# Performance work log

Measured on AMD Instinct MI355X. Metric: run time of the kernel, lower is better.

Reference implementation:

```python
import jax, jax.numpy as jnp
import numpy as np
from jax import lax

HID = 128  # hidden_dim
K = 2      # kernel (must be 2 for the torch slice arithmetic to be shape-consistent)


def skew(x):
    # x: (B,C,H,W) -> (B,C,H,2W-1), row r shifted right by r
    B, C, H, W = x.shape
    rows = jnp.arange(H)[:, None]
    cols = jnp.arange(W)[None, :] + rows
    y = jnp.zeros((B, C, H, 2 * W - 1), x.dtype)
    return y.at[:, :, rows, cols].set(x)


def unskew(x):
    B, C, H, Wp = x.shape
    W = (Wp + 1) // 2
    rows = jnp.arange(H)[:, None]
    cols = jnp.arange(W)[None, :] + rows
    return x[:, :, rows, cols]


def setup_inputs() -> dict:
    key = jax.random.key(0)
    k1, k2, k3 = jax.random.split(key, 3)
    Cin = 128
    x = jax.random.normal(k1, (8, Cin, 64, 64), jnp.float32)
    w_is = jax.random.normal(k2, (4 * HID, Cin), jnp.float32) * 0.05   # 1x1 conv weight
    b_is = jnp.zeros((4 * HID,), jnp.float32)
    w_ss = jax.random.normal(k3, (4 * HID, HID, K, 1), jnp.float32) * 0.05  # (k,1) conv weight
    b_ss = jnp.zeros((4 * HID,), jnp.float32)
    return {"x": x, "w_is": w_is, "b_is": b_is, "w_ss": w_ss, "b_ss": b_ss}


def reference(x, w_is, b_is, w_ss, b_ss):
    B, Cin, H, W = x.shape
    hid, k = HID, K
    xs = skew(x)  # (B,Cin,H,2W-1)
    # input-to-state: 1x1 conv (mask B on 1x1 kernel == plain 1x1 conv)
    z_is = jnp.einsum('bchw,oc->bohw', xs, w_is) + b_is[None, :, None, None]
    steps = z_is.transpose(3, 0, 1, 2)  # (2W-1, B, 4hid, H)

    h0 = jnp.zeros((B, hid, H), x.dtype)
    c0 = jnp.zeros((B, hid, H), x.dtype)

    def step(carry, z_t):
        h, c = carry  # (B,hid,H)
        # state-to-state (k,1) conv along H, padding k//2, then drop last k-1 rows
        hs = lax.conv_general_dilated(h[..., None], w_ss, (1, 1),
                                      [(k // 2, k // 2), (0, 0)],
                                      dimension_numbers=('NCHW', 'OIHW', 'NCHW'))
        hs = hs[:, :, :-(k - 1), 0] + b_ss[None, :, None]  # (B,4hid,H)
        z = z_t + hs
        i = jax.nn.sigmoid(z[:, :hid])
        f = jax.nn.sigmoid(z[:, hid:2 * hid])
        o = jax.nn.sigmoid(z[:, 2 * hid:3 * hid])
        g = jnp.tanh(z[:, 3 * hid:])
        c = f * c + i * g
        h = o * jnp.tanh(c)
        return (h, c), h

    _, hs_all = lax.scan(step, (h0, c0), steps)  # (2W-1,B,hid,H)
    out = hs_all.transpose(1, 2, 3, 0)  # (B,hid,H,2W-1)
    return unskew(out)  # (B,hid,H,W)
```

## Files before the change

kernel.cpp:

```cpp
#include <hip/hip_runtime.h>
#include <hip/hip_fp16.h>
#include <math.h>


#define HID 128
#define BB 8
#define HH 64
#define WW 64
#define TT 127

#define NPREP 1022

#define HROW 136

typedef _Float16 v8h __attribute__((ext_vector_type(8)));
typedef float v4f __attribute__((ext_vector_type(4)));

#define SENT64 0xFFFFFFFFFFFFFFFFULL

__device__ __forceinline__ float fsig(float x) {
  float e = __builtin_amdgcn_exp2f(x * -1.44269504f);
  return __builtin_amdgcn_rcpf(1.f + e);
}
__device__ __forceinline__ float ftanh_(float x) {
  float e = __builtin_amdgcn_exp2f(x * 2.88539009f);
  return __builtin_fmaf(-2.f, __builtin_amdgcn_rcpf(1.f + e), 1.f);
}

__global__ __launch_bounds__(256) void prep_k(
    const float* __restrict__ w_ss, const float* __restrict__ b_is,
    const float* __restrict__ b_ss, _Float16* __restrict__ wp,
    __half* __restrict__ zph, unsigned long long* __restrict__ hx) {
  int idx = blockIdx.x * 256 + threadIdx.x;
  if (idx < 131072) {
    int j = idx & 7;
    int L = (idx >> 3) & 63;
    int kt = (idx >> 9) & 7;
    int mt = idx >> 12;
    int O = mt * 16 + (L & 15);
    int k = kt * 32 + ((L >> 4) & 3) * 8 + j;
    float v = (k < 128) ? w_ss[(size_t)O * 256 + k * 2]
                        : w_ss[(size_t)O * 256 + (k - 128) * 2 + 1];
    wp[idx] = (_Float16)v;
  } else if (idx < 131584) {
    int idx2 = idx - 131072;
    int g = (idx2 >> 2) & 3;
    int u = (idx2 >> 4) * 4 + (idx2 & 3);
    int O = g * 128 + u;
    zph[(size_t)BB * HH * WW * 512 + idx2] = __float2half(b_is[O] + b_ss[O]);
  } else {
    int j = idx - 131584;
    uint4 s;
    s.x = 0xFFFFFFFFu; s.y = 0xFFFFFFFFu;
    s.z = 0xFFFFFFFFu; s.w = 0xFFFFFFFFu;
    ((uint4*)hx)[j] = s;
  }
}

#define STEP_BARRIER()                                   \
  do {                                                   \
    asm volatile("s_waitcnt lgkmcnt(0)" ::: "memory");   \
    __builtin_amdgcn_s_barrier();                        \
    asm volatile("" ::: "memory");                       \
  } while (0)

#define HPLD(p) __hip_atomic_load((p), __ATOMIC_RELAXED, __HIP_MEMORY_SCOPE_AGENT)

#define STEP_BODY(T, RB)                                                       \
  do {                                                                         \
           \
    v8h bfr[4];                                                                \
    _Pragma("unroll") for (int kt = 0; kt < 4; kt++)                           \
        bfr[kt] = *(const v8h*)&h_lds[RB][(rl * 2 + bl) * HROW + kt * 32 +     \
                                          quad * 8];                           \
                               \
    v4f zi[4];                                                                 \
    _Pragma("unroll") for (int g = 0; g < 4; g++)                              \
        _Pragma("unroll") for (int i = 0; i < 4; i++)                          \
        zi[g][i] = __half2float(zu.h[g * 4 + i]);                              \
         \
    {                                                                          \
      const uint4* p = (const uint4*)(((unsigned)wn < WW) ? zcur : zbias);     \
      zu.q[0] = p[0];                                                          \
      zu.q[1] = p[1];                                                          \
      wn++;                                                                    \
      zcur += 512;                                                             \
    }                                                                          \
          \
    v4f acc0[4], acc1[4];                                                      \
    _Pragma("unroll") for (int g = 0; g < 4; g++) {                            \
      acc0[g] = (v4f){0.f, 0.f, 0.f, 0.f};                                     \
      acc1[g] = zi[g];                                                         \
    }                                                                          \
    _Pragma("unroll") for (int kt = 0; kt < 4; kt++) {                         \
      _Pragma("unroll") for (int g = 0; g < 4; g++)                            \
          acc0[g] = __builtin_amdgcn_mfma_f32_16x16x32_f16(                    \
              wfrag[g][kt], bfr[kt], acc0[g], 0, 0, 0);                        \
    }                                                                          \
    _Pragma("unroll") for (int kt = 0; kt < 4; kt++) {                         \
      v8h bf1 = *(const v8h*)&h_lds[RB][((rl + 1) * 2 + bl) * HROW + kt * 32 + \
                                        quad * 8];                             \
      _Pragma("unroll") for (int g = 0; g < 4; g++)                            \
          acc1[g] = __builtin_amdgcn_mfma_f32_16x16x32_f16(                    \
              wfrag[g][4 + kt], bf1, acc1[g], 0, 0, 0);                        \
    }                                                                          \
         \
    unsigned long long pend = 0ull;                                            \
    if (is_cons) pend = HPLD(ca);                                              \
                        \
    const int w = (T)-r;                                                       \
    const bool inband = ((unsigned)w < WW);                                    \
    float hv[4];                                                               \
    _Pragma("unroll") for (int rg2 = 0; rg2 < 4; rg2++) {                      \
      float z0 = acc0[0][rg2] + acc1[0][rg2];                                  \
      float z1 = acc0[1][rg2] + acc1[1][rg2];                                  \
      float z2 = acc0[2][rg2] + acc1[2][rg2];                                  \
      float z3 = acc0[3][rg2] + acc1[3][rg2];                                  \
      float iv = fsig(z0);                                                     \
      float fv = fsig(z1);                                                     \
      float ov = fsig(z2);                                                     \
      float gv = ftanh_(z3);                                                   \
      c[rg2] = fv * c[rg2] + iv * gv;                                          \
      hv[rg2] = ov * ftanh_(c[rg2]);                                           \
    }                                                                          \
                       \
    __half2 plo = __floats2half2_rn(hv[0], hv[1]);                             \
    __half2 phi = __floats2half2_rn(hv[2], hv[3]);                             \
    {                                                                          \
      uint2 pk;                                                                \
      pk.x = *(unsigned*)&plo;                                                 \
      pk.y = *(unsigned*)&phi;                                                 \
      *(uint2*)&h_lds[(RB) ^ 1][((rl + 1) * 2 + bl) * HROW + uq0] = pk;        \
    }                                                                          \
              \
    if (rgr < 7 && l15 >= 14) {                                                \
      unsigned long long pk =                                                  \
          ((unsigned long long)*(unsigned*)&phi << 32) | *(unsigned*)&plo;     \
      __hip_atomic_store(pa_hx, pk, __ATOMIC_RELAXED,                          \
                         __HIP_MEMORY_SCOPE_AGENT);                            \
    }                                                                          \
    pa_hx += 2048;                                                             \
             \
    _Pragma("unroll") for (int rg2 = 0; rg2 < 4; rg2++) {                      \
      outb[rg2].x = outb[rg2].y;                                               \
      outb[rg2].y = outb[rg2].z;                                               \
      outb[rg2].z = outb[rg2].w;                                               \
      outb[rg2].w = hv[rg2];                                                   \
    }                                                                          \
    if (inband && (w & 3) == 3) {                                              \
      *(float4*)op0 = outb[0];                                                 \
      *(float4*)op1 = outb[1];                                                 \
      *(float4*)op2 = outb[2];                                                 \
      *(float4*)op3 = outb[3];                                                 \
      op0 += 4; op1 += 4; op2 += 4; op3 += 4;                                  \
    }                                                                          \
                          \
    if (is_cons) {                                                             \
      while (__ballot(pend == SENT64) != 0ull) {                               \
        __builtin_amdgcn_s_sleep(1);                                           \
        pend = HPLD(ca);                                                       \
      }                                                                        \
      *(unsigned long long*)&h_lds[(RB) ^ 1][(0 * 2 + ebl) * HROW + eu] =      \
          pend;                                                                \
    }                                                                          \
    ca += 2048;                                                                \
    STEP_BARRIER();                                                            \
  } while (0)

__global__ __launch_bounds__(512, 1) void lstm_mfma(
    const __half* __restrict__ zphc, const _Float16* __restrict__ wp,
    unsigned long long* __restrict__ hx,
    float* __restrict__ out, const float* __restrict__ x,
    const float* __restrict__ w_is, const float* __restrict__ b_is,
    const float* __restrict__ b_ss, __half* __restrict__ zphw) {
  const int blk = blockIdx.x;
  const int rgr = blk >> 2;
  const int bg = blk & 3;
  const int R0 = rgr * 8;
  const int tid = threadIdx.x;
  const int wv = tid >> 6;
  const int L = tid & 63;
  const int quad = L >> 4;
  const int l15 = L & 15;
  const int rl = l15 >> 1;
  const int bl = l15 & 1;
  const int b = bg * 2 + bl;
  const int r = R0 + rl;
  const int uq0 = 16 * wv + quad * 4;
  const int zoff = (4 * wv + quad) * 16;

  __shared__ _Float16 h_lds[2][9 * 2 * HROW];
  __shared__ _Float16 xt[64][136];
  for (int i = tid; i < (2 * 9 * 2 * HROW) / 2; i += 512)
    ((unsigned*)h_lds)[i] = 0u;

  {
    v8h wfr[4][4];
    float4 bvv[4];
#pragma unroll
    for (int m = 0; m < 4; m++) {
      const int mt = 4 * wv + m;
      const int O = mt * 16 + l15;
#pragma unroll
      for (int kt = 0; kt < 4; kt++) {
        const float* p = w_is + (size_t)O * 128 + kt * 32 + quad * 8;
        float4 a = *(const float4*)p;
        float4 b2 = *(const float4*)(p + 4);
        v8h f;
        f[0] = (_Float16)a.x;  f[1] = (_Float16)a.y;
        f[2] = (_Float16)a.z;  f[3] = (_Float16)a.w;
        f[4] = (_Float16)b2.x; f[5] = (_Float16)b2.y;
        f[6] = (_Float16)b2.z; f[7] = (_Float16)b2.w;
        wfr[m][kt] = f;
      }
      const int O4 = mt * 16 + quad * 4;
      float4 bi = *(const float4*)&b_is[O4];
      float4 bs4 = *(const float4*)&b_ss[O4];
      bvv[m] = make_float4(bi.x + bs4.x, bi.y + bs4.y, bi.z + bs4.z,
                           bi.w + bs4.w);
    }

    for (int tt = 0; tt < 16; tt++) {
      const int b2 = bg * 2 + (tt & 1);
      const int r2 = R0 + (tt >> 1);
      __syncthreads();
      {
        const int cw = tid >> 4;
        const int w4 = (tid & 15) * 4;
#pragma unroll
        for (int p = 0; p < 4; p++) {
          int cc = p * 32 + cw;
          float4 v =
              *(const float4*)&x[(((size_t)b2 * 128 + cc) * HH + r2) * WW + w4];
          xt[w4 + 0][cc] = (_Float16)v.x;
          xt[w4 + 1][cc] = (_Float16)v.y;
          xt[w4 + 2][cc] = (_Float16)v.z;
          xt[w4 + 3][cc] = (_Float16)v.w;
        }
      }
      __syncthreads();
#pragma unroll
      for (int nt = 0; nt < 4; nt++) {
        v8h bf[4];
#pragma unroll
        for (int kt = 0; kt < 4; kt++)
          bf[kt] = *(const v8h*)&xt[nt * 16 + l15][kt * 32 + quad * 8];
        const size_t pos = ((size_t)b2 * HH + r2) * WW + nt * 16 + l15;
#pragma unroll
        for (int m = 0; m < 4; m++) {
          v4f acc = (v4f){0.f, 0.f, 0.f, 0.f};
#pragma unroll
          for (int kt = 0; kt < 4; kt++)
            acc = __builtin_amdgcn_mfma_f32_16x16x32_f16(wfr[m][kt], bf[kt],
                                                         acc, 0, 0, 0);
          const int mt = 4 * wv + m;
          __half2 lo = __floats2half2_rn(acc[0] + bvv[m].x, acc[1] + bvv[m].y);
          __half2 hi = __floats2half2_rn(acc[2] + bvv[m].z, acc[3] + bvv[m].w);
          uint2 pk;
          pk.x = *(unsigned*)&lo;
          pk.y = *(unsigned*)&hi;
          *(uint2*)&zphw[pos * 512 + ((mt & 7) * 4 + quad) * 16 +
                         (mt >> 3) * 4] = pk;
        }
      }
    }
    asm volatile("s_waitcnt vmcnt(0)" ::: "memory");
    __syncthreads();
  }
  const __half* zph = zphc;

  v8h wfrag[4][8];
  {
    const v8h* wp8 = (const v8h*)wp;
#pragma unroll
    for (int g = 0; g < 4; g++)
#pragma unroll
      for (int kt = 0; kt < 8; kt++)
        wfrag[g][kt] = wp8[((size_t)((8 * g + wv) * 8 + kt)) * 64 + L];
  }

  float c[4] = {0.f, 0.f, 0.f, 0.f};
  float4 outb[4];
#pragma unroll
  for (int i = 0; i < 4; i++) outb[i] = make_float4(0.f, 0.f, 0.f, 0.f);

  const int ebl = L >> 5;
  const int eu = (L & 31) * 4;
  const int exp_idx = bl * 32 + 4 * wv + quad;

  const bool is_cons = (wv == 0) && (rgr > 0);

  const __half* zpp = zph + ((size_t)b * HH + r) * WW * 512 + zoff;
  const __half* zbias = zph + (size_t)BB * HH * WW * 512 + zoff;
  const unsigned long long* ca =
      hx + (((size_t)(rgr > 0 ? rgr - 1 : 0) * 4 + bg) * 64 + L);
  unsigned long long* pa_hx = hx + (((size_t)rgr * 4 + bg) * 64 + exp_idx);
  float* op0 = out + (((size_t)b * HID + uq0 + 0) * HH + r) * WW;
  float* op1 = out + (((size_t)b * HID + uq0 + 1) * HH + r) * WW;
  float* op2 = out + (((size_t)b * HID + uq0 + 2) * HH + r) * WW;
  float* op3 = out + (((size_t)b * HID + uq0 + 3) * HH + r) * WW;

  union ZU {
    uint4 q[2];
    __half h[16];
  } zu;
  {
    const uint4* p0 = (const uint4*)((r == 0) ? zpp : zbias);
    zu.q[0] = p0[0];
    zu.q[1] = p0[1];
  }
  int wn = 1 - r;
  const __half* zcur = zpp + (ptrdiff_t)wn * 512;

  __syncthreads();

  for (int t = 0; t < TT - 1; t += 2) {
    STEP_BODY(t, 0);
    STEP_BODY(t + 1, 1);
  }
  STEP_BODY(TT - 1, 0);
}

__global__ __launch_bounds__(256) void transpose_x(const float* __restrict__ x,
                                                   float* __restrict__ xT) {
  int b = blockIdx.x >> 6;
  int r = blockIdx.x & 63;
  __shared__ float tile[32][65];
  for (int cc = 0; cc < 4; cc++) {
    int cl = threadIdx.x >> 6;
    int w = threadIdx.x & 63;
#pragma unroll
    for (int k = 0; k < 8; k++) {
      int c_loc = k * 4 + cl;
      int c = cc * 32 + c_loc;
      tile[c_loc][w] = x[(((size_t)b * 128 + c) * HH + r) * WW + w];
    }
    __syncthreads();
    int cs = threadIdx.x & 31;
    int wp = threadIdx.x >> 5;
#pragma unroll
    for (int k = 0; k < 8; k++) {
      int w2 = wp * 8 + k;
      xT[(((size_t)b * HH + r) * WW + w2) * 128 + cc * 32 + cs] = tile[cs][w2];
    }
    __syncthreads();
  }
}

__global__ __launch_bounds__(256) void step_kernel(
    const float* __restrict__ x, const float* __restrict__ xT, int use_xT,
    const float* __restrict__ w_is, const float* __restrict__ b_is,
    const float* __restrict__ w_ss, const float* __restrict__ b_ss,
    const float* __restrict__ h_prev, float* __restrict__ h_next,
    float* __restrict__ c_state, float* __restrict__ out, int t) {
  const int rg = blockIdx.x;
  const int q = blockIdx.y;
  const int r0 = rg * 2;
  const int tid = threadIdx.x;
  const int o_loc = tid & 63;
  const int k4 = tid >> 6;
  const int g_ = o_loc >> 4;
  const int u_ = o_loc & 15;
  const int O = g_ * 128 + q * 16 + u_;
  const int i0 = k4 * 32;

  __shared__ __align__(16) float h_in[3][BB][HID];
  __shared__ float zred[16][4][65];

  for (int idx = tid; idx < 3 * BB * HID; idx += 256) {
    int row_sel = idx >> 10;
    int rem = idx & 1023;
    int b = rem >> 7;
    int u = rem & 127;
    int rr = r0 - 1 + row_sel;
    h_in[row_sel][b][u] = (rr >= 0) ? h_prev[((size_t)b * HH + rr) * HID + u] : 0.0f;
  }

  float wr0[32], wr1[32], wz[32];
  {
    const float4* wss4 = (const float4*)(w_ss + ((size_t)O * 128 + i0) * 2);
#pragma unroll
    for (int j = 0; j < 16; j++) {
      float4 v = wss4[j];
      wr0[2 * j] = v.x;
      wr1[2 * j] = v.y;
      wr0[2 * j + 1] = v.z;
      wr1[2 * j + 1] = v.w;
    }
    const float4* wis4 = (const float4*)(w_is + (size_t)O * 128 + i0);
#pragma unroll
    for (int j = 0; j < 8; j++) {
      float4 v = wis4[j];
      wz[4 * j] = v.x;
      wz[4 * j + 1] = v.y;
      wz[4 * j + 2] = v.z;
      wz[4 * j + 3] = v.w;
    }
  }

  __syncthreads();

  float acc[2][BB];
#pragma unroll
  for (int rl = 0; rl < 2; rl++)
#pragma unroll
    for (int b = 0; b < BB; b++) acc[rl][b] = 0.0f;

#pragma unroll
  for (int jb = 0; jb < 8; jb++) {
    int ib = i0 + jb * 4;
#pragma unroll
    for (int b = 0; b < BB; b++) {
      const float4 hm4 = *(const float4*)&h_in[0][b][ib];
      const float4 hc4 = *(const float4*)&h_in[1][b][ib];
      const float4 hp4 = *(const float4*)&h_in[2][b][ib];
      const float* hm = (const float*)&hm4;
      const float* hc = (const float*)&hc4;
      const float* hq = (const float*)&hp4;
#pragma unroll
      for (int jj = 0; jj < 4; jj++) {
        float w0v = wr0[jb * 4 + jj];
        float w1v = wr1[jb * 4 + jj];
        acc[0][b] += w0v * hm[jj] + w1v * hc[jj];
        acc[1][b] += w0v * hc[jj] + w1v * hq[jj];
      }
    }
  }

#pragma unroll
  for (int rl = 0; rl < 2; rl++) {
    int rr = r0 + rl;
    int wcol = t - rr;
    if (wcol >= 0 && wcol < WW) {
      if (use_xT) {
        for (int b = 0; b < BB; b++) {
          const float4* xp =
              (const float4*)(xT + (((size_t)b * HH + rr) * WW + wcol) * 128 + i0);
#pragma unroll
          for (int j = 0; j < 8; j++) {
            float4 v = xp[j];
            acc[rl][b] += wz[4 * j] * v.x + wz[4 * j + 1] * v.y +
                          wz[4 * j + 2] * v.z + wz[4 * j + 3] * v.w;
          }
        }
      } else {
        for (int b = 0; b < BB; b++) {
          const float* xb = x + (((size_t)b * 128 + i0) * HH + rr) * WW + wcol;
#pragma unroll
          for (int j = 0; j < 32; j++) {
            acc[rl][b] += wz[j] * xb[(size_t)j * HH * WW];
          }
        }
      }
    }
  }

#pragma unroll
  for (int rl = 0; rl < 2; rl++)
#pragma unroll
    for (int b = 0; b < BB; b++) zred[rl * 8 + b][k4][o_loc] = acc[rl][b];
  __syncthreads();

  {
    int u = tid >> 4;
    int cell = tid & 15;
    int rl = cell >> 3;
    int b = cell & 7;
    int rr = r0 + rl;
    float z[4];
#pragma unroll
    for (int gg = 0; gg < 4; gg++) {
      int ol = gg * 16 + u;
      float s = zred[cell][0][ol] + zred[cell][1][ol] + zred[cell][2][ol] +
                zred[cell][3][ol];
      int Og = gg * 128 + q * 16 + u;
      z[gg] = s + b_is[Og] + b_ss[Og];
    }
    float iv = 1.0f / (1.0f + expf(-z[0]));
    float fv = 1.0f / (1.0f + expf(-z[1]));
    float ov = 1.0f / (1.0f + expf(-z[2]));
    float gv = tanhf(z[3]);
    int U = q * 16 + u;
    size_t sidx = ((size_t)b * HH + rr) * HID + U;
    float cv = c_state[sidx];
    float cn = fv * cv + iv * gv;
    c_state[sidx] = cn;
    float hn = ov * tanhf(cn);
    h_next[sidx] = hn;
    int wcol = t - rr;
    if (wcol >= 0 && wcol < WW) {
      out[(((size_t)b * HID + U) * HH + rr) * WW + wcol] = hn;
    }
  }
}

extern "C" void kernel_launch(void* const* d_in, const int* in_sizes, int n_in,
                              void* d_out, int out_size, void* d_ws,
                              size_t ws_size, hipStream_t stream) {
  const float* x = (const float*)d_in[0];
  const float* w_is = (const float*)d_in[1];
  const float* b_is = (const float*)d_in[2];
  const float* w_ss = (const float*)d_in[3];
  const float* b_ss = (const float*)d_in[4];
  float* outp = (float*)d_out;

  const size_t zph_bytes = ((size_t)BB * HH * WW * 512 + 512) * 2;
  const size_t wp_bytes = (size_t)512 * 256 * 2;
  const size_t hx_bytes = (size_t)TT * 8 * 4 * 64 * 8;
  const size_t need = zph_bytes + wp_bytes + hx_bytes;

  char* ws = (char*)d_ws;
  if (ws_size >= need) {
    __half* zph = (__half*)ws;
    _Float16* wpp = (_Float16*)(ws + zph_bytes);
    unsigned long long* hx =
        (unsigned long long*)(ws + zph_bytes + wp_bytes);

    prep_k<<<dim3(NPREP), 256, 0, stream>>>(w_ss, b_is, b_ss, wpp, zph, hx);
    lstm_mfma<<<dim3(32), 512, 0, stream>>>(zph, wpp, hx, outp, x, w_is,
                                            b_is, b_ss, zph);
  } else {
    const size_t xT_elems = (size_t)BB * HH * WW * 128;
    const size_t st_elems = (size_t)BB * HH * HID;
    const size_t need_xT = (xT_elems + 3 * st_elems) * sizeof(float);
    float* wsf = (float*)d_ws;
    float* xT = nullptr;
    float* st;
    int use_xT = 0;
    if (ws_size >= need_xT) {
      use_xT = 1;
      xT = wsf;
      st = wsf + xT_elems;
    } else {
      st = wsf;
    }
    float* h0 = st;
    float* h1 = st + st_elems;
    float* cb = st + 2 * st_elems;
    hipMemsetAsync(st, 0, 3 * st_elems * sizeof(float), stream);
    if (use_xT) transpose_x<<<dim3(BB * HH), 256, 0, stream>>>(x, xT);
    for (int t = 0; t < TT; t++) {
      float* hp = (t & 1) ? h1 : h0;
      float* hn = (t & 1) ? h0 : h1;
      step_kernel<<<dim3(32, 8), 256, 0, stream>>>(x, xT, use_xT, w_is, b_is,
                                                   w_ss, b_ss, hp, hn, cb, outp,
                                                   t);
    }
  }
}
```

Measured before the change: 359.5 us.

## Offload input projection to separate producer blocks with per-row ready flags

Before, the 32 recurrent blocks each computed their share of the input-to-state projection serially before starting the scan. The input projection now runs in 512 extra producer blocks, one per (row, batch), launched in the same grid. Each producer sets a per-(row, batch) flag with release semantics. Recurrent blocks spin on their flag, with an acquire fence, before first reading z for that row, which spreads the projection across the GPU and lets it overlap the wavefront start. The cost is a dependency on producers getting scheduled alongside the persistent blocks (a deadlock risk if they cannot co-reside), plus spin-wait overhead.

Result: faster. 322.0 us (-10.4%).

```diff
diff --git a/kernel.cpp b/kernel.cpp
--- a/kernel.cpp
+++ b/kernel.cpp
@@ -9,7 +9,7 @@
 #define WW 64
 #define TT 127
 
-#define NPREP 1022
+#define NPREP 1024
 
 #define HROW 136
 
@@ -30,7 +30,8 @@
 __global__ __launch_bounds__(256) void prep_k(
     const float* __restrict__ w_ss, const float* __restrict__ b_is,
     const float* __restrict__ b_ss, _Float16* __restrict__ wp,
-    __half* __restrict__ zph, unsigned long long* __restrict__ hx) {
+    __half* __restrict__ zph, unsigned* __restrict__ zflag,
+    unsigned long long* __restrict__ hx) {
   int idx = blockIdx.x * 256 + threadIdx.x;
   if (idx < 131072) {
     int j = idx & 7;
@@ -48,8 +49,10 @@
     int u = (idx2 >> 4) * 4 + (idx2 & 3);
     int O = g * 128 + u;
     zph[(size_t)BB * HH * WW * 512 + idx2] = __float2half(b_is[O] + b_ss[O]);
+  } else if (idx < 132096) {
+    zflag[idx - 131584] = 0u;
   } else {
-    int j = idx - 131584;
+    int j = idx - 132096;
     uint4 s;
     s.x = 0xFFFFFFFFu; s.y = 0xFFFFFFFFu;
     s.z = 0xFFFFFFFFu; s.w = 0xFFFFFFFFu;
@@ -78,8 +81,15 @@
     _Pragma("unroll") for (int g = 0; g < 4; g++)                              \
         _Pragma("unroll") for (int i = 0; i < 4; i++)                          \
         zi[g][i] = __half2float(zu.h[g * 4 + i]);                              \
-         \
+        \
     {                                                                          \
+      if (!zdone && (unsigned)wn < WW) {                                       \
+        while (__hip_atomic_load(zf, __ATOMIC_RELAXED,                         \
+                                 __HIP_MEMORY_SCOPE_AGENT) == 0u)              \
+          __builtin_amdgcn_s_sleep(2);                                         \
+        __builtin_amdgcn_fence(__ATOMIC_ACQUIRE, "agent");                     \
+        zdone = true;                                                          \
+      }                                                                        \
       const uint4* p = (const uint4*)(((unsigned)wn < WW) ? zcur : zbias);     \
       zu.q[0] = p[0];                                                          \
       zu.q[1] = p[1];                                                          \
@@ -167,39 +177,47 @@
     STEP_BARRIER();                                                            \
   } while (0)
 
-__global__ __launch_bounds__(512, 1) void lstm_mfma(
-    const __half* __restrict__ zphc, const _Float16* __restrict__ wp,
-    unsigned long long* __restrict__ hx,
-    float* __restrict__ out, const float* __restrict__ x,
-    const float* __restrict__ w_is, const float* __restrict__ b_is,
-    const float* __restrict__ b_ss, __half* __restrict__ zphw) {
+__global__ __launch_bounds__(512, 1) void fused(
+    const __half* __restrict__ zph, const _Float16* __restrict__ wp,
+    unsigned long long* __restrict__ hx, float* __restrict__ out,
+    const float* __restrict__ x, const float* __restrict__ w_is,
+    const float* __restrict__ b_is, const float* __restrict__ b_ss,
+    unsigned* __restrict__ zflag, __half* __restrict__ zphw) {
+  __shared__ _Float16 h_lds[2][9 * 2 * HROW];
+  __shared__ _Float16 xt[64][136];
+
   const int blk = blockIdx.x;
-  const int rgr = blk >> 2;
-  const int bg = blk & 3;
-  const int R0 = rgr * 8;
   const int tid = threadIdx.x;
-  const int wv = tid >> 6;
   const int L = tid & 63;
   const int quad = L >> 4;
   const int l15 = L & 15;
-  const int rl = l15 >> 1;
-  const int bl = l15 & 1;
-  const int b = bg * 2 + bl;
-  const int r = R0 + rl;
-  const int uq0 = 16 * wv + quad * 4;
-  const int zoff = (4 * wv + quad) * 16;
-
-  __shared__ _Float16 h_lds[2][9 * 2 * HROW];
-  __shared__ _Float16 xt[64][136];
-  for (int i = tid; i < (2 * 9 * 2 * HROW) / 2; i += 512)
-    ((unsigned*)h_lds)[i] = 0u;
-
-  {
+
+  if (blk >= 32) {
+    const int i = blk - 32;
+    const int r = i >> 3;
+    const int b = i & 7;
+    const int wv8 = tid >> 6;
+
+    {
+      const int cw = tid >> 4;
+      const int w4 = (tid & 15) * 4;
+#pragma unroll
+      for (int p = 0; p < 4; p++) {
+        int cc = p * 32 + cw;
+        float4 v =
+            *(const float4*)&x[(((size_t)b * 128 + cc) * HH + r) * WW + w4];
+        xt[w4 + 0][cc] = (_Float16)v.x;
+        xt[w4 + 1][cc] = (_Float16)v.y;
+        xt[w4 + 2][cc] = (_Float16)v.z;
+        xt[w4 + 3][cc] = (_Float16)v.w;
+      }
+    }
+
     v8h wfr[4][4];
     float4 bvv[4];
 #pragma unroll
     for (int m = 0; m < 4; m++) {
-      const int mt = 4 * wv + m;
+      const int mt = 4 * wv8 + m;
       const int O = mt * 16 + l15;
 #pragma unroll
       for (int kt = 0; kt < 4; kt++) {
@@ -220,54 +238,55 @@
                            bi.w + bs4.w);
     }
 
-    for (int tt = 0; tt < 16; tt++) {
-      const int b2 = bg * 2 + (tt & 1);
-      const int r2 = R0 + (tt >> 1);
-      __syncthreads();
-      {
-        const int cw = tid >> 4;
-        const int w4 = (tid & 15) * 4;
-#pragma unroll
-        for (int p = 0; p < 4; p++) {
-          int cc = p * 32 + cw;
-          float4 v =
-              *(const float4*)&x[(((size_t)b2 * 128 + cc) * HH + r2) * WW + w4];
-          xt[w4 + 0][cc] = (_Float16)v.x;
-          xt[w4 + 1][cc] = (_Float16)v.y;
-          xt[w4 + 2][cc] = (_Float16)v.z;
-          xt[w4 + 3][cc] = (_Float16)v.w;
-        }
+    __syncthreads();
+
+#pragma unroll
+    for (int nt = 0; nt < 4; nt++) {
+      v8h bf[4];
+#pragma unroll
+      for (int kt = 0; kt < 4; kt++)
+        bf[kt] = *(const v8h*)&xt[nt * 16 + l15][kt * 32 + quad * 8];
+      const size_t pos = ((size_t)b * HH + r) * WW + nt * 16 + l15;
+#pragma unroll
+      for (int m = 0; m < 4; m++) {
+        v4f acc = (v4f){0.f, 0.f, 0.f, 0.f};
+#pragma unroll
+        for (int kt = 0; kt < 4; kt++)
+          acc = __builtin_amdgcn_mfma_f32_16x16x32_f16(wfr[m][kt], bf[kt], acc,
+                                                       0, 0, 0);
+        const int mt = 4 * wv8 + m;
+        __half2 lo = __floats2half2_rn(acc[0] + bvv[m].x, acc[1] + bvv[m].y);
+        __half2 hi = __floats2half2_rn(acc[2] + bvv[m].z, acc[3] + bvv[m].w);
+        uint2 pk;
+        pk.x = *(unsigned*)&lo;
+        pk.y = *(unsigned*)&hi;
+        *(uint2*)&zphw[pos * 512 + ((mt & 7) * 4 + quad) * 16 +
+                       (mt >> 3) * 4] = pk;
       }
-      __syncthreads();
-#pragma unroll
-      for (int nt = 0; nt < 4; nt++) {
-        v8h bf[4];
-#pragma unroll
-        for (int kt = 0; kt < 4; kt++)
-          bf[kt] = *(const v8h*)&xt[nt * 16 + l15][kt * 32 + quad * 8];
-        const size_t pos = ((size_t)b2 * HH + r2) * WW + nt * 16 + l15;
-#pragma unroll
-        for (int m = 0; m < 4; m++) {
-          v4f acc = (v4f){0.f, 0.f, 0.f, 0.f};
-#pragma unroll
-          for (int kt = 0; kt < 4; kt++)
-            acc = __builtin_amdgcn_mfma_f32_16x16x32_f16(wfr[m][kt], bf[kt],
-                                                         acc, 0, 0, 0);
-          const int mt = 4 * wv + m;
-          __half2 lo = __floats2half2_rn(acc[0] + bvv[m].x, acc[1] + bvv[m].y);
-          __half2 hi = __floats2half2_rn(acc[2] + bvv[m].z, acc[3] + bvv[m].w);
-          uint2 pk;
-          pk.x = *(unsigned*)&lo;
-          pk.y = *(unsigned*)&hi;
-          *(uint2*)&zphw[pos * 512 + ((mt & 7) * 4 + quad) * 16 +
-                         (mt >> 3) * 4] = pk;
-        }
-      }
-    }
-    asm volatile("s_waitcnt vmcnt(0)" ::: "memory");
+    }
+
     __syncthreads();
-  }
-  const __half* zph = zphc;
+    if (tid == 0) {
+      __builtin_amdgcn_fence(__ATOMIC_RELEASE, "agent");
+      __hip_atomic_store(&zflag[i], 1u, __ATOMIC_RELAXED,
+                         __HIP_MEMORY_SCOPE_AGENT);
+    }
+    return;
+  }
+
+  const int rgr = blk >> 2;
+  const int bg = blk & 3;
+  const int R0 = rgr * 8;
+  const int wv = tid >> 6;
+  const int rl = l15 >> 1;
+  const int bl = l15 & 1;
+  const int b = bg * 2 + bl;
+  const int r = R0 + rl;
+  const int uq0 = 16 * wv + quad * 4;
+  const int zoff = (4 * wv + quad) * 16;
+
+  for (int i = tid; i < (2 * 9 * 2 * HROW) / 2; i += 512)
+    ((unsigned*)h_lds)[i] = 0u;
 
   v8h wfrag[4][8];
   {
@@ -300,11 +319,21 @@
   float* op2 = out + (((size_t)b * HID + uq0 + 2) * HH + r) * WW;
   float* op3 = out + (((size_t)b * HID + uq0 + 3) * HH + r) * WW;
 
+  unsigned* zf = &zflag[r * 8 + b];
+  bool zdone = false;
+
   union ZU {
     uint4 q[2];
     __half h[16];
   } zu;
   {
+    if (r == 0) {
+      while (__hip_atomic_load(zf, __ATOMIC_RELAXED,
+                               __HIP_MEMORY_SCOPE_AGENT) == 0u)
+        __builtin_amdgcn_s_sleep(2);
+      __builtin_amdgcn_fence(__ATOMIC_ACQUIRE, "agent");
+      zdone = true;
+    }
     const uint4* p0 = (const uint4*)((r == 0) ? zpp : zbias);
     zu.q[0] = p0[0];
     zu.q[1] = p0[1];
@@ -507,7 +536,8 @@
   const size_t zph_bytes = ((size_t)BB * HH * WW * 512 + 512) * 2;
   const size_t wp_bytes = (size_t)512 * 256 * 2;
   const size_t hx_bytes = (size_t)TT * 8 * 4 * 64 * 8;
-  const size_t need = zph_bytes + wp_bytes + hx_bytes;
+  const size_t zflag_bytes = 512 * sizeof(unsigned);
+  const size_t need = zph_bytes + wp_bytes + hx_bytes + zflag_bytes;
 
   char* ws = (char*)d_ws;
   if (ws_size >= need) {
@@ -515,10 +545,12 @@
     _Float16* wpp = (_Float16*)(ws + zph_bytes);
     unsigned long long* hx =
         (unsigned long long*)(ws + zph_bytes + wp_bytes);
-
-    prep_k<<<dim3(NPREP), 256, 0, stream>>>(w_ss, b_is, b_ss, wpp, zph, hx);
-    lstm_mfma<<<dim3(32), 512, 0, stream>>>(zph, wpp, hx, outp, x, w_is,
-                                            b_is, b_ss, zph);
+    unsigned* zflag = (unsigned*)(ws + zph_bytes + wp_bytes + hx_bytes);
+
+    prep_k<<<dim3(NPREP), 256, 0, stream>>>(w_ss, b_is, b_ss, wpp, zph,
+                                            zflag, hx);
+    fused<<<dim3(544), 512, 0, stream>>>(zph, wpp, hx, outp, x, w_is, b_is,
+                                         b_ss, zflag, zph);
   } else {
     const size_t xT_elems = (size_t)BB * HH * WW * 128;
     const size_t st_elems = (size_t)BB * HH * HID;
```
